# Performance work log

Hardware: AMD Instinct MI355X
Metric: run time of the kernel (lower is better)

## Reference

```python
import jax, jax.numpy as jnp
import numpy as np

B, S, D, H, Dh, A_N = 2, 1024, 512, 8, 64, 18
HID = H * Dh        # 512, equals in_features
FFN = 4 * D         # SwiGLU hidden (ratio=4)
EPS = 1e-6


def rmsnorm(x, scale):
    return x * jax.lax.rsqrt(jnp.mean(jnp.square(x), axis=-1, keepdims=True) + EPS) * scale


def setup_inputs() -> dict:
    key = jax.random.key(0)
    ks = jax.random.split(key, 16)
    lecun = lambda k, shp: jax.random.normal(k, shp, jnp.float32) * (1.0 / np.sqrt(shp[0]))
    return {
        "x": jax.random.normal(ks[0], (B, S, D), jnp.float32),
        "action": jax.random.randint(ks[1], (B, S), 0, A_N, jnp.int32),
        "mask": jnp.zeros((B, S), jnp.int32),
        "carry": jnp.zeros((B, H, Dh, Dh), jnp.float32),
        "norm1_scale": jnp.ones((D,), jnp.float32),
        "wq": lecun(ks[2], (D, HID)),
        "wk": lecun(ks[3], (D, HID)),
        "wv": lecun(ks[4], (D, HID)),
        "w_beta": lecun(ks[5], (D, H)),
        "embed": jax.random.normal(ks[6], (A_N, HID), jnp.float32) * 0.02,
        "w_alpha": lecun(ks[7], (HID, H)),
        "w_bu": lecun(ks[8], (HID, HID)),
        "w_bv": lecun(ks[9], (HID, HID)),
        "norm_attn_scale": jnp.ones((HID,), jnp.float32),
        "w_out": lecun(ks[10], (HID, D)),
        "b_out": jnp.zeros((D,), jnp.float32),
        "norm2_scale": jnp.ones((D,), jnp.float32),
        "w_gate": lecun(ks[11], (D, FFN)),
        "w_val": lecun(ks[12], (D, FFN)),
        "w_ffn": lecun(ks[13], (FFN, D)),
    }


def reference(x, action, mask, carry, norm1_scale, wq, wk, wv, w_beta, embed,
              w_alpha, w_bu, w_bv, norm_attn_scale, w_out, b_out,
              norm2_scale, w_gate, w_val, w_ffn):
    dt = x.dtype
    h = rmsnorm(x, norm1_scale)
    # projections -> [B,S,H,Dh]
    q = jax.nn.silu(h @ wq).reshape(B, S, H, Dh)
    k = jax.nn.silu(h @ wk).reshape(B, S, H, Dh)
    v = (h @ wv).reshape(B, S, H, Dh)
    beta = jax.nn.sigmoid(h @ w_beta)                       # [B,S,H]
    ae = embed[action]                                      # [B,S,HID]
    alpha = jax.nn.sigmoid(ae @ w_alpha)                    # [B,S,H]
    b_u = (ae @ w_bu).reshape(B, S, H, Dh)
    b_v = (ae @ w_bv).reshape(B, S, H, Dh)
    q = q / (jnp.linalg.norm(q, axis=-1, keepdims=True) + EPS)
    k = k / (jnp.linalg.norm(k, axis=-1, keepdims=True) + EPS)
    eye = jnp.eye(Dh, dtype=dt)
    # delta = I - beta * k k^T   -> [B,S,H,Dh,Dh]
    delta = eye - beta[..., None, None] * jnp.einsum("bshi,bshj->bshij", k, k)
    m = mask.astype(dt)[:, :, None, None, None]
    decay = alpha[..., None, None] * delta * (1.0 - m)
    drift = jnp.einsum("bshi,bshj->bshij", b_u, b_v)
    write = beta[..., None, None] * jnp.einsum("bshi,bshj->bshij", v, k)
    update = drift @ delta + write

    def binop(lhs, rhs):
        a_i, b_i = lhs
        a_j, b_j = rhs
        return (a_i @ a_j, b_i @ a_j + b_j)

    cumdecay, hs = jax.lax.associative_scan(jax.vmap(binop), (decay, update), axis=1)
    hs = carry[:, None] @ cumdecay + hs                     # [B,S,H,Dh,Dh]
    attn = jnp.einsum("bshij,bshj->bshi", hs, q).reshape(B, S, HID)
    attn = rmsnorm(attn, norm_attn_scale)
    y = attn @ w_out + b_out
    skip = y + x
    h2 = rmsnorm(skip, norm2_scale)
    ffn = (jax.nn.silu(h2 @ w_gate) * (h2 @ w_val)) @ w_ffn
    return (hs[:, -1], skip + ffn)
```

## Files before the change

### kernel.cpp

```cpp
#include <hip/hip_runtime.h>
#include <hip/hip_bf16.h>
#include <cstdint>
#include <cstddef>

using bf16 = __hip_bfloat16;
typedef __attribute__((ext_vector_type(8))) short bf16x8;
typedef __attribute__((ext_vector_type(4))) float f32x4;

static constexpr int B_ = 2, S_ = 1024, D_ = 512, H_ = 8;
static constexpr int M_ = B_ * S_;
static constexpr int CHUNKS_ = 64, CLEN_ = 16;
static constexpr float EPS_ = 1e-6f;

__device__ __forceinline__ float sigmoidf_(float x) { return 1.0f / (1.0f + __expf(-x)); }

__device__ __forceinline__ short bf_hi(float v, float& rem) {
  bf16 h = __float2bfloat16(v);
  rem = v - __bfloat162float(h);
  return *(short*)&h;
}
__device__ __forceinline__ short bf_of(float v) {
  bf16 h = __float2bfloat16(v);
  return *(short*)&h;
}

struct TJob { const float* src; bf16* dst; int K, N, base, xf; };
struct TTab { TJob j[9]; };

__global__ __launch_bounds__(256) void k_transpose_all(TTab tab) {
  __shared__ float tile[32][33];
  int blk = blockIdx.x;
  int ji = 0;
#pragma unroll
  for (int t = 1; t < 9; ++t) if (tab.j[t].base <= blk) ji = t;
  const float* W = tab.j[ji].src;
  bf16* Wt = tab.j[ji].dst;
  int K = tab.j[ji].K, N = tab.j[ji].N, xf = tab.j[ji].xf;
  int rel = blk - tab.j[ji].base;
  int nb = N >> 5;
  int n0 = (rel % nb) * 32, k0 = (rel / nb) * 32;
  int tx = threadIdx.x, ty = threadIdx.y;
#pragma unroll
  for (int r = ty; r < 32; r += 8) tile[r][tx] = W[(size_t)(k0 + r) * N + n0 + tx];
  __syncthreads();
#pragma unroll
  for (int r = ty; r < 32; r += 8) {
    int n = n0 + r;
    int drow = n;
    if (xf == 1) drow = ((n >> 5) << 6) + (n & 31);
    else if (xf == 2) drow = ((n >> 5) << 6) + (n & 31) + 32;
    Wt[(size_t)drow * K + k0 + tx] = __float2bfloat16(tile[tx][r]);
  }
}

__global__ __launch_bounds__(256) void k_pre(const float* __restrict__ x,
                                             const float* __restrict__ scale,
                                             float* __restrict__ hF, bf16* __restrict__ hB,
                                             const int* __restrict__ action,
                                             const float* __restrict__ embed,
                                             float* __restrict__ aeF, bf16* __restrict__ aeB) {
  int tid = threadIdx.x;
  if (blockIdx.x < M_) {
    int m = blockIdx.x;
    const float* row = x + (size_t)m * D_;
    float2 v = *(const float2*)(row + tid * 2);
    float ss = v.x * v.x + v.y * v.y;
#pragma unroll
    for (int o = 1; o < 64; o <<= 1) ss += __shfl_xor(ss, o);
    __shared__ float wsum[4];
    if ((tid & 63) == 0) wsum[tid >> 6] = ss;
    __syncthreads();
    float tot = wsum[0] + wsum[1] + wsum[2] + wsum[3];
    float rs = rsqrtf(tot * (1.0f / (float)D_) + EPS_);
    float2 sc = *(const float2*)(scale + tid * 2);
    float o0 = v.x * rs * sc.x, o1 = v.y * rs * sc.y;
    float2 o; o.x = o0; o.y = o1;
    *(float2*)(hF + (size_t)m * D_ + tid * 2) = o;
    bf16* p = hB + (size_t)m * D_ + tid * 2;
    p[0] = __float2bfloat16(o0); p[1] = __float2bfloat16(o1);
  } else {
    int m = blockIdx.x - M_;
    int a = action[m];
    float2 v = *(const float2*)(embed + (size_t)a * 512 + tid * 2);
    *(float2*)(aeF + (size_t)m * 512 + tid * 2) = v;
    bf16* p = aeB + (size_t)m * 512 + tid * 2;
    p[0] = __float2bfloat16(v.x); p[1] = __float2bfloat16(v.y);
  }
}

__global__ __launch_bounds__(256) void k_rmsnorm(const float* __restrict__ x,
                                                 const float* __restrict__ scale,
                                                 float* __restrict__ outf,
                                                 bf16* __restrict__ outb) {
  int m = blockIdx.x, tid = threadIdx.x;
  const float* row = x + (size_t)m * D_;
  float2 v = *(const float2*)(row + tid * 2);
  float ss = v.x * v.x + v.y * v.y;
#pragma unroll
  for (int o = 1; o < 64; o <<= 1) ss += __shfl_xor(ss, o);
  __shared__ float wsum[4];
  if ((tid & 63) == 0) wsum[tid >> 6] = ss;
  __syncthreads();
  float tot = wsum[0] + wsum[1] + wsum[2] + wsum[3];
  float rs = rsqrtf(tot * (1.0f / (float)D_) + EPS_);
  float2 sc = *(const float2*)(scale + tid * 2);
  float o0 = v.x * rs * sc.x, o1 = v.y * rs * sc.y;
  if (outf) {
    float2 o; o.x = o0; o.y = o1;
    *(float2*)(outf + (size_t)m * D_ + tid * 2) = o;
  }
  if (outb) {
    bf16* p = outb + (size_t)m * D_ + tid * 2;
    p[0] = __float2bfloat16(o0); p[1] = __float2bfloat16(o1);
  }
}

__global__ __launch_bounds__(256) void k_dot8x2(const float* __restrict__ hF,
                                                const float* __restrict__ aeF,
                                                const float* __restrict__ W1,
                                                const float* __restrict__ W2,
                                                float* __restrict__ o1,
                                                float* __restrict__ o2) {
  int m = blockIdx.x, tid = threadIdx.x;
  float x0 = hF[(size_t)m * D_ + tid], x1 = hF[(size_t)m * D_ + 256 + tid];
  float y0 = aeF[(size_t)m * D_ + tid], y1 = aeF[(size_t)m * D_ + 256 + tid];
  float p[8], q[8];
#pragma unroll
  for (int j = 0; j < 8; ++j) {
    p[j] = x0 * W1[tid * 8 + j] + x1 * W1[(tid + 256) * 8 + j];
    q[j] = y0 * W2[tid * 8 + j] + y1 * W2[(tid + 256) * 8 + j];
  }
#pragma unroll
  for (int j = 0; j < 8; ++j) {
#pragma unroll
    for (int o = 1; o < 64; o <<= 1) {
      p[j] += __shfl_xor(p[j], o);
      q[j] += __shfl_xor(q[j], o);
    }
  }
  __shared__ float sacc[4][16];
  if ((tid & 63) == 0) {
#pragma unroll
    for (int j = 0; j < 8; ++j) { sacc[tid >> 6][j] = p[j]; sacc[tid >> 6][8 + j] = q[j]; }
  }
  __syncthreads();
  if (tid < 8) {
    float s = sacc[0][tid] + sacc[1][tid] + sacc[2][tid] + sacc[3][tid];
    o1[(size_t)m * 8 + tid] = sigmoidf_(s);
  } else if (tid < 16) {
    int j = tid - 8;
    float s = sacc[0][8 + j] + sacc[1][8 + j] + sacc[2][8 + j] + sacc[3][8 + j];
    o2[(size_t)m * 8 + j] = sigmoidf_(s);
  }
}

__global__ __launch_bounds__(256) void k_qknorm_dots(float* __restrict__ qkv,
                                                     const float* __restrict__ buv,
                                                     const float* __restrict__ betaF,
                                                     const float* __restrict__ alphaF,
                                                     const int* __restrict__ mask,
                                                     float* __restrict__ scal8) {
  int blk = blockIdx.x * 4 + (threadIdx.x >> 6);
  int m = blk >> 3, h = blk & 7, t = threadIdx.x & 63;
  size_t qi = (size_t)m * 1536 + h * 64 + t;
  float q = qkv[qi], k = qkv[qi + 512];
  float bv = buv[(size_t)m * 1024 + 512 + h * 64 + t];
  float qs = q * q, ks = k * k;
#pragma unroll
  for (int o = 1; o < 64; o <<= 1) { qs += __shfl_xor(qs, o); ks += __shfl_xor(ks, o); }
  float qn = q / (sqrtf(qs) + EPS_);
  float kn = k / (sqrtf(ks) + EPS_);
  qkv[qi] = qn; qkv[qi + 512] = kn;
  float d0 = kn * qn, d1 = kn * bv, d2 = bv * qn;
#pragma unroll
  for (int o = 1; o < 64; o <<= 1) {
    d0 += __shfl_xor(d0, o); d1 += __shfl_xor(d1, o); d2 += __shfl_xor(d2, o);
  }
  if (t == 0) {
    int mh = m * 8 + h;
    float4 s4;
    s4.x = betaF[mh];
    s4.y = alphaF[mh] * (1.0f - (float)mask[m]);
    s4.z = d0; s4.w = d1;
    *(float4*)(scal8 + (size_t)mh * 8) = s4;
    scal8[(size_t)mh * 8 + 4] = d2;
  }
}

template <int EPI>
__global__ __launch_bounds__(256) void k_gemm2(const bf16* __restrict__ A,
                                               const bf16* __restrict__ Bt,
                                               void* __restrict__ Cv, int M, int N, int K,
                                               int actSplit, const float* __restrict__ bias,
                                               const float* __restrict__ res) {
  __shared__ bf16 As[2][64 * 32];
  __shared__ bf16 Bs[2][64 * 32];
  const int tid = threadIdx.x;
  const int wave = tid >> 6, lane = tid & 63;
  const int wm = wave >> 1, wn = wave & 1;
  const int m0 = blockIdx.y * 64, n0 = blockIdx.x * 64;
  const int lr = lane & 15, lg = lane >> 4;
  const int srow = (wave << 4) | (lane >> 2);
  const int skb = (lane & 3) << 3;
  const bf16* ga = A + (size_t)(m0 + srow) * K + skb;
  const bf16* gb = Bt + (size_t)(n0 + srow) * K + skb;

  f32x4 acc[2][2];
#pragma unroll
  for (int i = 0; i < 2; ++i)
#pragma unroll
    for (int j = 0; j < 2; ++j) acc[i][j] = (f32x4){0.f, 0.f, 0.f, 0.f};

  const int nk = K >> 5;
  int4 ar = *(const int4*)ga;
  int4 br = *(const int4*)gb;
  for (int t = 0; t < nk; ++t) {
    bf16* asb = &As[t & 1][0];
    bf16* bsb = &Bs[t & 1][0];
    *(int4*)(asb + tid * 8) = ar;
    *(int4*)(bsb + tid * 8) = br;
    __syncthreads();
    if (t + 1 < nk) {
      ar = *(const int4*)(ga + ((size_t)(t + 1) << 5));
      br = *(const int4*)(gb + ((size_t)(t + 1) << 5));
    }
    bf16x8 af[2], bfr[2];
#pragma unroll
    for (int mm = 0; mm < 2; ++mm)
      af[mm] = *(const bf16x8*)(asb + (wm * 32 + mm * 16 + lr) * 32 + lg * 8);
#pragma unroll
    for (int nn = 0; nn < 2; ++nn)
      bfr[nn] = *(const bf16x8*)(bsb + (wn * 32 + nn * 16 + lr) * 32 + lg * 8);
#pragma unroll
    for (int mm = 0; mm < 2; ++mm)
#pragma unroll
      for (int nn = 0; nn < 2; ++nn)
        acc[mm][nn] = __builtin_amdgcn_mfma_f32_16x16x32_bf16(af[mm], bfr[nn], acc[mm][nn], 0, 0, 0);
  }

  if constexpr (EPI == 4) {
    __syncthreads();
    float* gateL = (float*)&As[0][0];
    float* valL = (float*)&Bs[0][0];
    float* dstL = wn ? valL : gateL;
#pragma unroll
    for (int mm = 0; mm < 2; ++mm)
#pragma unroll
      for (int nn = 0; nn < 2; ++nn)
#pragma unroll
        for (int r = 0; r < 4; ++r)
          dstL[(wm * 32 + mm * 16 + lg * 4 + r) * 32 + nn * 16 + lr] = acc[mm][nn][r];
    __syncthreads();
    bf16* Cb = (bf16*)Cv;
    int row = tid >> 2, c0 = (tid & 3) * 8;
    bf16x8 o;
#pragma unroll
    for (int e = 0; e < 8; ++e) {
      float g = gateL[row * 32 + c0 + e];
      float v = valL[row * 32 + c0 + e];
      o[e] = bf_of(g * sigmoidf_(g) * v);
    }
    *(int4*)(Cb + (size_t)(m0 + row) * 2048 + blockIdx.x * 32 + c0) = *(int4*)&o;
  } else {
    float* C = (float*)Cv;
#pragma unroll
    for (int mm = 0; mm < 2; ++mm) {
#pragma unroll
      for (int nn = 0; nn < 2; ++nn) {
#pragma unroll
        for (int r = 0; r < 4; ++r) {
          int row = m0 + wm * 32 + mm * 16 + lg * 4 + r;
          int col = n0 + wn * 32 + nn * 16 + lr;
          float v = acc[mm][nn][r];
          if constexpr (EPI == 1) {
            if (col < actSplit) v = v * sigmoidf_(v);
          }
          if constexpr (EPI == 2) v += bias[col] + res[(size_t)row * N + col];
          if constexpr (EPI == 3) v += res[(size_t)row * N + col];
          C[(size_t)row * N + col] = v;
        }
      }
    }
  }
}


__global__ __launch_bounds__(512) void k_scan_chunk(
    const float* __restrict__ qkv, const float* __restrict__ buv,
    const float* __restrict__ scal8, bf16* __restrict__ PtHi,
    bf16* __restrict__ PtLo, float* __restrict__ Ut,
    float* __restrict__ Qtb, float* __restrict__ Vtb) {
  __shared__ float kL[CLEN_][64], qL[CLEN_][64], bvL[CLEN_][64];
  __shared__ float vL[CLEN_][64], buL[CLEN_][64];
  __shared__ float scL[CLEN_][8];
  const int blk = blockIdx.x, bh = blk >> 6, c = blk & (CHUNKS_ - 1);
  const int b = bh >> 3, h = bh & 7;
  const int tid = threadIdx.x, i = tid >> 3, q8 = tid & 7, j0 = q8 * 8;
  const bool writer = (q8 == 0);
  const int m0 = b * S_ + c * CLEN_;

  if (tid < 256) {
    int s = tid >> 4, fo = (tid & 15) * 4;
    const float* qb = qkv + (size_t)(m0 + s) * 1536 + h * 64;
    const float* bb = buv + (size_t)(m0 + s) * 1024 + h * 64;
    *(float4*)&qL[s][fo]  = *(const float4*)(qb + fo);
    *(float4*)&kL[s][fo]  = *(const float4*)(qb + 512 + fo);
    *(float4*)&vL[s][fo]  = *(const float4*)(qb + 1024 + fo);
    *(float4*)&buL[s][fo] = *(const float4*)(bb + fo);
    *(float4*)&bvL[s][fo] = *(const float4*)(bb + 512 + fo);
    if ((tid & 15) < 2)
      *(float4*)&scL[s][(tid & 1) * 4] =
          *(const float4*)(scal8 + (size_t)((m0 + s) * 8 + h) * 8 + (tid & 1) * 4);
  }
  __syncthreads();

  alignas(16) float P[8], U[8];
#pragma unroll
  for (int jj = 0; jj < 8; ++jj) { P[jj] = (j0 + jj == i) ? 1.f : 0.f; U[jj] = 0.f; }
  float* QT = Qtb + ((size_t)bh * CHUNKS_ + c) * (CLEN_ * 64);
  float* VT = Vtb + ((size_t)bh * CHUNKS_ + c) * (CLEN_ * 64);

  struct Step8 { float k[8], q[8], bv[8]; float v_i, bu_i, beta, g, kq, kbv, bvq; };
  auto LOAD = [&](Step8& sd, int s) {
    *(float4*)&sd.k[0]  = *(const float4*)&kL[s][j0];
    *(float4*)&sd.k[4]  = *(const float4*)&kL[s][j0 + 4];
    *(float4*)&sd.q[0]  = *(const float4*)&qL[s][j0];
    *(float4*)&sd.q[4]  = *(const float4*)&qL[s][j0 + 4];
    *(float4*)&sd.bv[0] = *(const float4*)&bvL[s][j0];
    *(float4*)&sd.bv[4] = *(const float4*)&bvL[s][j0 + 4];
    sd.v_i = vL[s][i];
    sd.bu_i = buL[s][i];
    float4 s4 = *(const float4*)&scL[s][0];
    sd.beta = s4.x; sd.g = s4.y; sd.kq = s4.z; sd.kbv = s4.w;
    sd.bvq = scL[s][4];
  };
  auto STEP = [&](const Step8& sd, int s) {
    float Pk = 0.f, Uk = 0.f, Pq = 0.f, Uq = 0.f;
#pragma unroll
    for (int jj = 0; jj < 8; ++jj) {
      Pk += P[jj] * sd.k[jj]; Uk += U[jj] * sd.k[jj];
      Pq += P[jj] * sd.q[jj]; Uq += U[jj] * sd.q[jj];
    }
    Pk += __shfl_xor(Pk, 1); Pk += __shfl_xor(Pk, 2); Pk += __shfl_xor(Pk, 4);
    Uk += __shfl_xor(Uk, 1); Uk += __shfl_xor(Uk, 2); Uk += __shfl_xor(Uk, 4);
    Pq += __shfl_xor(Pq, 1); Pq += __shfl_xor(Pq, 2); Pq += __shfl_xor(Pq, 4);
    Uq += __shfl_xor(Uq, 1); Uq += __shfl_xor(Uq, 2); Uq += __shfl_xor(Uq, 4);
    float gb = sd.g * sd.beta;
    float cP = gb * Pk;
    float Ai = sd.beta * sd.v_i - gb * Uk - sd.bu_i * sd.beta * sd.kbv;
    if (writer) {
      QT[s * 64 + i] = sd.g * Pq - cP * sd.kq;
      VT[s * 64 + i] = sd.g * Uq + Ai * sd.kq + sd.bu_i * sd.bvq;
    }
#pragma unroll
    for (int jj = 0; jj < 8; ++jj) {
      P[jj] = sd.g * P[jj] - cP * sd.k[jj];
      U[jj] = sd.g * U[jj] + Ai * sd.k[jj] + sd.bu_i * sd.bv[jj];
    }
  };

  Step8 A, Bs;
  LOAD(A, 0);
  LOAD(Bs, 1);
  for (int s = 0; s < CLEN_; s += 2) {
    STEP(A, s);
    if (s + 2 < CLEN_) LOAD(A, s + 2);
    STEP(Bs, s + 1);
    if (s + 3 < CLEN_) LOAD(Bs, s + 3);
  }

  const size_t base = ((size_t)bh * CHUNKS_ + c) * 4096;
#pragma unroll
  for (int jj = 0; jj < 8; ++jj) {
    int j = j0 + jj;
    float pv = P[jj];
    float rem;
    short ph = bf_hi(pv, rem);
    short pl = bf_of(rem);
    ((short*)PtHi)[base + (size_t)j * 64 + i] = ph;
    ((short*)PtLo)[base + (size_t)j * 64 + i] = pl;
    Ut[base + (size_t)j * 64 + i] = U[jj];
  }
}

#define PREFETCH_(SET, CIDX)                                                     \
  {                                                                              \
    const size_t cbo_ = (size_t)(CIDX) * 4096;                                   \
    _Pragma("unroll") for (int mt = 0; mt < 4; ++mt) {                           \
      _Pragma("unroll") for (int ks = 0; ks < 2; ++ks) {                         \
        size_t off_ = cbo_ + (size_t)(16 * mt + lr) * 64 + ks * 32 + lg * 8;     \
        aH[SET][mt][ks] = *(const bf16x8*)(PH + off_);                           \
        aL[SET][mt][ks] = *(const bf16x8*)(PL + off_);                           \
      }                                                                          \
      _Pragma("unroll") for (int r = 0; r < 4; ++r)                              \
        u[SET][mt][r] = UB[cbo_ + (size_t)(16 * mt + 4 * lg + r) * 64 + col0 + lr]; \
    }                                                                            \
  }

#define CHAINSTEP_(SET, NSET, CIDX)                                              \
  {                                                                              \
    if ((CIDX) + 1 < CHUNKS_) PREFETCH_(NSET, (CIDX) + 1);                       \
    _Pragma("unroll") for (int mt = 0; mt < 4; ++mt)                             \
      _Pragma("unroll") for (int r = 0; r < 4; ++r)                              \
        HB[(size_t)(CIDX) * 4096 + (size_t)(16 * mt + 4 * lg + r) * 64 + col0 + lr] = st[mt][r]; \
    bf16x8 bH[2], bL[2];                                                         \
    _Pragma("unroll") for (int ks = 0; ks < 2; ++ks) {                           \
      _Pragma("unroll") for (int e = 0; e < 8; ++e) {                            \
        int src_ = (2 * (lg & 1) + (e >> 2)) * 16 + lr;                          \
        float va_ = __shfl(st[2 * ks][e & 3], src_);                             \
        float vb_ = __shfl(st[2 * ks + 1][e & 3], src_);                         \
        float bv_ = (lg & 2) ? vb_ : va_;                                        \
        float rem_;                                                              \
        bH[ks][e] = bf_hi(bv_, rem_);                                            \
        bL[ks][e] = bf_of(rem_);                                                 \
      }                                                                          \
    }                                                                            \
    f32x4 stn[4];                                                                \
    _Pragma("unroll") for (int mt = 0; mt < 4; ++mt) {                           \
      f32x4 a_ = u[SET][mt];                                                     \
      _Pragma("unroll") for (int ks = 0; ks < 2; ++ks) {                         \
        a_ = __builtin_amdgcn_mfma_f32_16x16x32_bf16(aH[SET][mt][ks], bH[ks], a_, 0, 0, 0); \
        a_ = __builtin_amdgcn_mfma_f32_16x16x32_bf16(aH[SET][mt][ks], bL[ks], a_, 0, 0, 0); \
        a_ = __builtin_amdgcn_mfma_f32_16x16x32_bf16(aL[SET][mt][ks], bH[ks], a_, 0, 0, 0); \
      }                                                                          \
      stn[mt] = a_;                                                              \
    }                                                                            \
    _Pragma("unroll") for (int mt = 0; mt < 4; ++mt) st[mt] = stn[mt];           \
  }

__global__ __launch_bounds__(64, 1) void k_chain3(
    const bf16* __restrict__ PtHi, const bf16* __restrict__ PtLo,
    const float* __restrict__ Ut, const float* __restrict__ carry,
    float* __restrict__ Hbuf, float* __restrict__ out_hs) {
  const int bh = blockIdx.x >> 2, cb = blockIdx.x & 3, col0 = cb * 16;
  const int lane = threadIdx.x & 63, lr = lane & 15, lg = lane >> 4;
  const short* PH = (const short*)PtHi + (size_t)bh * CHUNKS_ * 4096;
  const short* PL = (const short*)PtLo + (size_t)bh * CHUNKS_ * 4096;
  const float* UB = Ut + (size_t)bh * CHUNKS_ * 4096;
  float* HB = Hbuf + (size_t)bh * CHUNKS_ * 4096;

  f32x4 st[4];
#pragma unroll
  for (int mt = 0; mt < 4; ++mt)
    st[mt] = *(const f32x4*)(carry + ((size_t)bh * 64 + col0 + lr) * 64 + 16 * mt + 4 * lg);

  bf16x8 aH[2][4][2], aL[2][4][2];
  f32x4 u[2][4];
  PREFETCH_(0, 0);
  for (int c = 0; c < CHUNKS_; c += 2) {
    CHAINSTEP_(0, 1, c);
    CHAINSTEP_(1, 0, c + 1);
  }
#pragma unroll
  for (int mt = 0; mt < 4; ++mt)
    *(f32x4*)(out_hs + ((size_t)bh * 64 + col0 + lr) * 64 + 16 * mt + 4 * lg) = st[mt];
}

__global__ __launch_bounds__(256) void k_attn_gemm(
    const float* __restrict__ Hbuf, const float* __restrict__ Qtb,
    const float* __restrict__ Vtb, float* __restrict__ attn) {
  const int blk = blockIdx.x, bh = blk >> 6, c = blk & (CHUNKS_ - 1);
  const int b = bh >> 3, h = bh & 7;
  const int tid = threadIdx.x, wave = tid >> 6, lane = tid & 63;
  const int lr = lane & 15, lg = lane >> 4;
  const float* H0 = Hbuf + ((size_t)bh * CHUNKS_ + c) * 4096;
  const float* QT = Qtb + ((size_t)bh * CHUNKS_ + c) * (CLEN_ * 64);
  const float* VT = Vtb + ((size_t)bh * CHUNKS_ + c) * (CLEN_ * 64);

  bf16x8 aH[2], aL[2];
#pragma unroll
  for (int ks = 0; ks < 2; ++ks) {
#pragma unroll
    for (int e = 0; e < 8; ++e) {
      float v = H0[(size_t)(ks * 32 + lg * 8 + e) * 64 + wave * 16 + lr];
      float rem;
      aH[ks][e] = bf_hi(v, rem);
      aL[ks][e] = bf_of(rem);
    }
  }
  f32x4 a = (f32x4){0.f, 0.f, 0.f, 0.f};
#pragma unroll
  for (int ks = 0; ks < 2; ++ks) {
    const float* qp = QT + (size_t)lr * 64 + ks * 32 + lg * 8;
    bf16x8 bH, bL;
#pragma unroll
    for (int e = 0; e < 8; ++e) {
      float rem;
      bH[e] = bf_hi(qp[e], rem);
      bL[e] = bf_of(rem);
    }
    a = __builtin_amdgcn_mfma_f32_16x16x32_bf16(aH[ks], bH, a, 0, 0, 0);
    a = __builtin_amdgcn_mfma_f32_16x16x32_bf16(aH[ks], bL, a, 0, 0, 0);
    a = __builtin_amdgcn_mfma_f32_16x16x32_bf16(aL[ks], bH, a, 0, 0, 0);
  }
  const int m0 = b * S_ + c * CLEN_;
  {
    int s = lr;
    f32x4 vt = *(const f32x4*)(VT + (size_t)s * 64 + wave * 16 + lg * 4);
#pragma unroll
    for (int r = 0; r < 4; ++r) a[r] += vt[r];
    *(f32x4*)(attn + (size_t)(m0 + s) * 512 + h * 64 + wave * 16 + lg * 4) = a;
  }
}

extern "C" void kernel_launch(void* const* d_in, const int* in_sizes, int n_in,
                              void* d_out, int out_size, void* d_ws, size_t ws_size,
                              hipStream_t stream) {
  const float* x      = (const float*)d_in[0];
  const int*   action = (const int*)d_in[1];
  const int*   mask   = (const int*)d_in[2];
  const float* carry  = (const float*)d_in[3];
  const float* n1s    = (const float*)d_in[4];
  const float* wq     = (const float*)d_in[5];
  const float* wk     = (const float*)d_in[6];
  const float* wv     = (const float*)d_in[7];
  const float* wbeta  = (const float*)d_in[8];
  const float* embed  = (const float*)d_in[9];
  const float* walpha = (const float*)d_in[10];
  const float* wbu    = (const float*)d_in[11];
  const float* wbv    = (const float*)d_in[12];
  const float* nas    = (const float*)d_in[13];
  const float* wout   = (const float*)d_in[14];
  const float* bout   = (const float*)d_in[15];
  const float* n2s    = (const float*)d_in[16];
  const float* wgate  = (const float*)d_in[17];
  const float* wval   = (const float*)d_in[18];
  const float* wffn   = (const float*)d_in[19];

  float* out_hs  = (float*)d_out;
  float* out_ffn = (float*)d_out + 65536;

  char* p = (char*)d_ws;
  auto alloc = [&](size_t bytes) -> char* {
    char* r = p; p += (bytes + 255) & ~(size_t)255; return r;
  };
  bf16*  wqkvT = (bf16*)alloc((size_t)1536 * 512 * 2);
  bf16*  wbuvT = (bf16*)alloc((size_t)1024 * 512 * 2);
  bf16*  woutT = (bf16*)alloc((size_t)512 * 512 * 2);
  bf16*  wgvT  = (bf16*)alloc((size_t)4096 * 512 * 2);
  bf16*  wffnT = (bf16*)alloc((size_t)512 * 2048 * 2);
  float* qkvF  = (float*)alloc((size_t)M_ * 1536 * 4);
  float* buvF  = (float*)alloc((size_t)M_ * 1024 * 4);
  float* betaF = (float*)alloc((size_t)M_ * 8 * 4);
  float* alphaF= (float*)alloc((size_t)M_ * 8 * 4);
  float* scal8 = (float*)alloc((size_t)M_ * 8 * 8 * 4);
  float* attnF = (float*)alloc((size_t)M_ * 512 * 4);
  bf16*  attnB = (bf16*)alloc((size_t)M_ * 512 * 2);
  float* skipF = (float*)alloc((size_t)M_ * 512 * 4);
  bf16*  h2B   = (bf16*)alloc((size_t)M_ * 512 * 2);
  bf16*  ffnB  = (bf16*)alloc((size_t)M_ * 2048 * 2);
  char*  tail  = alloc((size_t)32 * 1024 * 1024);
  if ((size_t)(p - (char*)d_ws) > ws_size) return;

  float* hF  = (float*)tail;
  bf16*  hB  = (bf16*)(tail + ((size_t)4 << 20));
  float* aeF = (float*)(tail + ((size_t)6 << 20));
  bf16*  aeB = (bf16*)(tail + ((size_t)10 << 20));

  bf16*  PtHi = (bf16*)tail;
  bf16*  PtLo = (bf16*)(tail + ((size_t)8 << 20));
  float* UtB  = (float*)(tail + ((size_t)16 << 20));
  float* Hbuf = qkvF;
  float* Qtb  = (float*)attnB;
  float* Vtb  = (float*)((char*)skipF + ((size_t)2 << 20));

  TTab tab;
  tab.j[0] = {wq,    wqkvT,              512,  512,  0,    0};
  tab.j[1] = {wk,    wqkvT + 512 * 512,  512,  512,  256,  0};
  tab.j[2] = {wv,    wqkvT + 1024 * 512, 512,  512,  512,  0};
  tab.j[3] = {wbu,   wbuvT,              512,  512,  768,  0};
  tab.j[4] = {wbv,   wbuvT + 512 * 512,  512,  512,  1024, 0};
  tab.j[5] = {wout,  woutT,              512,  512,  1280, 0};
  tab.j[6] = {wgate, wgvT,               512,  2048, 1536, 1};
  tab.j[7] = {wval,  wgvT,               512,  2048, 2560, 2};
  tab.j[8] = {wffn,  wffnT,              2048, 512,  3584, 0};
  k_transpose_all<<<4608, dim3(32, 8), 0, stream>>>(tab);

  k_pre<<<M_ * 2, 256, 0, stream>>>(x, n1s, hF, hB, action, embed, aeF, aeB);

  k_gemm2<1><<<dim3(1536 / 64, M_ / 64), 256, 0, stream>>>(hB, wqkvT, qkvF, M_, 1536, 512, 1024, nullptr, nullptr);
  k_gemm2<0><<<dim3(1024 / 64, M_ / 64), 256, 0, stream>>>(aeB, wbuvT, buvF, M_, 1024, 512, 0, nullptr, nullptr);
  k_dot8x2<<<M_, 256, 0, stream>>>(hF, aeF, wbeta, walpha, betaF, alphaF);
  k_qknorm_dots<<<M_ * 2, 256, 0, stream>>>(qkvF, buvF, betaF, alphaF, mask, scal8);

  k_scan_chunk<<<16 * CHUNKS_, 512, 0, stream>>>(qkvF, buvF, scal8, PtHi, PtLo, UtB, Qtb, Vtb);
  k_chain3<<<64, 64, 0, stream>>>(PtHi, PtLo, UtB, carry, Hbuf, out_hs);
  k_attn_gemm<<<16 * CHUNKS_, 256, 0, stream>>>(Hbuf, Qtb, Vtb, attnF);

  k_rmsnorm<<<M_, 256, 0, stream>>>(attnF, nas, nullptr, attnB);
  k_gemm2<2><<<dim3(512 / 64, M_ / 64), 256, 0, stream>>>(attnB, woutT, skipF, M_, 512, 512, 0, bout, x);
  k_rmsnorm<<<M_, 256, 0, stream>>>(skipF, n2s, nullptr, h2B);
  k_gemm2<4><<<dim3(4096 / 64, M_ / 64), 256, 0, stream>>>(h2B, wgvT, ffnB, M_, 4096, 512, 0, nullptr, nullptr);
  k_gemm2<3><<<dim3(512 / 64, M_ / 64), 256, 0, stream>>>(ffnB, wffnT, out_ffn, M_, 512, 2048, 0, nullptr, skipF);
}
```

Baseline: 221.8 us.

## Use 16x16x16 MFMA in chain kernel to drop cross-lane shuffles

```diff
diff --git a/kernel.cpp b/kernel.cpp
--- a/kernel.cpp
+++ b/kernel.cpp
@@ -5,6 +5,7 @@
 
 using bf16 = __hip_bfloat16;
 typedef __attribute__((ext_vector_type(8))) short bf16x8;
+typedef __attribute__((ext_vector_type(4))) short short4v;
 typedef __attribute__((ext_vector_type(4))) float f32x4;
 
 static constexpr int B_ = 2, S_ = 1024, D_ = 512, H_ = 8;
@@ -383,77 +384,83 @@
   }
 }
 
-#define PREFETCH_(SET, CIDX)                                                     \
-  {                                                                              \
-    const size_t cbo_ = (size_t)(CIDX) * 4096;                                   \
-    _Pragma("unroll") for (int mt = 0; mt < 4; ++mt) {                           \
-      _Pragma("unroll") for (int ks = 0; ks < 2; ++ks) {                         \
-        size_t off_ = cbo_ + (size_t)(16 * mt + lr) * 64 + ks * 32 + lg * 8;     \
-        aH[SET][mt][ks] = *(const bf16x8*)(PH + off_);                           \
-        aL[SET][mt][ks] = *(const bf16x8*)(PL + off_);                           \
-      }                                                                          \
-      _Pragma("unroll") for (int r = 0; r < 4; ++r)                              \
-        u[SET][mt][r] = UB[cbo_ + (size_t)(16 * mt + 4 * lg + r) * 64 + col0 + lr]; \
-    }                                                                            \
-  }
-
-#define CHAINSTEP_(SET, NSET, CIDX)                                              \
-  {                                                                              \
-    if ((CIDX) + 1 < CHUNKS_) PREFETCH_(NSET, (CIDX) + 1);                       \
-    _Pragma("unroll") for (int mt = 0; mt < 4; ++mt)                             \
-      _Pragma("unroll") for (int r = 0; r < 4; ++r)                              \
-        HB[(size_t)(CIDX) * 4096 + (size_t)(16 * mt + 4 * lg + r) * 64 + col0 + lr] = st[mt][r]; \
-    bf16x8 bH[2], bL[2];                                                         \
-    _Pragma("unroll") for (int ks = 0; ks < 2; ++ks) {                           \
-      _Pragma("unroll") for (int e = 0; e < 8; ++e) {                            \
-        int src_ = (2 * (lg & 1) + (e >> 2)) * 16 + lr;                          \
-        float va_ = __shfl(st[2 * ks][e & 3], src_);                             \
-        float vb_ = __shfl(st[2 * ks + 1][e & 3], src_);                         \
-        float bv_ = (lg & 2) ? vb_ : va_;                                        \
-        float rem_;                                                              \
-        bH[ks][e] = bf_hi(bv_, rem_);                                            \
-        bL[ks][e] = bf_of(rem_);                                                 \
-      }                                                                          \
-    }                                                                            \
-    f32x4 stn[4];                                                                \
-    _Pragma("unroll") for (int mt = 0; mt < 4; ++mt) {                           \
-      f32x4 a_ = u[SET][mt];                                                     \
-      _Pragma("unroll") for (int ks = 0; ks < 2; ++ks) {                         \
-        a_ = __builtin_amdgcn_mfma_f32_16x16x32_bf16(aH[SET][mt][ks], bH[ks], a_, 0, 0, 0); \
-        a_ = __builtin_amdgcn_mfma_f32_16x16x32_bf16(aH[SET][mt][ks], bL[ks], a_, 0, 0, 0); \
-        a_ = __builtin_amdgcn_mfma_f32_16x16x32_bf16(aL[SET][mt][ks], bH[ks], a_, 0, 0, 0); \
-      }                                                                          \
-      stn[mt] = a_;                                                              \
-    }                                                                            \
-    _Pragma("unroll") for (int mt = 0; mt < 4; ++mt) st[mt] = stn[mt];           \
-  }
-
-__global__ __launch_bounds__(64, 1) void k_chain3(
+#define MFMA16_(Af, Bf, Cf) __builtin_amdgcn_mfma_f32_16x16x16bf16_1k(Af, Bf, Cf, 0, 0, 0)
+
+#define PF16_(SET, CIDX)                                                       \
+  {                                                                            \
+    const size_t pbo_ = (size_t)(CIDX) * 4096;                                 \
+    _Pragma("unroll") for (int mt = 0; mt < 4; ++mt)                           \
+      _Pragma("unroll") for (int kt = 0; kt < 4; ++kt) {                       \
+        size_t off_ = pbo_ + (size_t)(16 * mt + lr) * 64 + 16 * kt + 4 * lg;   \
+        aH[SET][mt][kt] = *(const short4v*)(PH + off_);                        \
+        aL[SET][mt][kt] = *(const short4v*)(PL + off_);                        \
+      }                                                                        \
+  }
+
+#define CS16_(SET, NSET, CIDX)                                                 \
+  {                                                                            \
+    if ((CIDX) + 1 < CHUNKS_) PF16_(NSET, (CIDX) + 1);                         \
+    const size_t cbo_ = (size_t)(CIDX) * 4096;                                 \
+    f32x4 u_[2][4];                                                            \
+    _Pragma("unroll") for (int ct = 0; ct < 2; ++ct)                           \
+      _Pragma("unroll") for (int mt = 0; mt < 4; ++mt)                         \
+        _Pragma("unroll") for (int r = 0; r < 4; ++r)                          \
+          u_[ct][mt][r] = UB[cbo_ + (size_t)(16 * mt + 4 * lg + r) * 64 + col0 + 16 * ct + lr]; \
+    short4v bH[2][4], bL[2][4];                                                \
+    _Pragma("unroll") for (int ct = 0; ct < 2; ++ct)                           \
+      _Pragma("unroll") for (int kt = 0; kt < 4; ++kt)                         \
+        _Pragma("unroll") for (int e = 0; e < 4; ++e) {                        \
+          float rem_;                                                          \
+          bH[ct][kt][e] = bf_hi(st[ct][kt][e], rem_);                          \
+          bL[ct][kt][e] = bf_of(rem_);                                         \
+        }                                                                      \
+    _Pragma("unroll") for (int ct = 0; ct < 2; ++ct)                           \
+      _Pragma("unroll") for (int kt = 0; kt < 4; ++kt)                         \
+        _Pragma("unroll") for (int r = 0; r < 4; ++r)                          \
+          HB[cbo_ + (size_t)(16 * kt + 4 * lg + r) * 64 + col0 + 16 * ct + lr] = st[ct][kt][r]; \
+    _Pragma("unroll") for (int ct = 0; ct < 2; ++ct)                           \
+      _Pragma("unroll") for (int mt = 0; mt < 4; ++mt) {                       \
+        f32x4 a_ = u_[ct][mt];                                                 \
+        _Pragma("unroll") for (int kt = 0; kt < 4; ++kt) {                     \
+          a_ = MFMA16_(aH[SET][mt][kt], bH[ct][kt], a_);                       \
+          a_ = MFMA16_(aH[SET][mt][kt], bL[ct][kt], a_);                       \
+          a_ = MFMA16_(aL[SET][mt][kt], bH[ct][kt], a_);                       \
+        }                                                                      \
+        st[ct][mt] = a_;                                                       \
+      }                                                                        \
+  }
+
+__global__ __launch_bounds__(64, 1) void k_chain4(
     const bf16* __restrict__ PtHi, const bf16* __restrict__ PtLo,
     const float* __restrict__ Ut, const float* __restrict__ carry,
     float* __restrict__ Hbuf, float* __restrict__ out_hs) {
-  const int bh = blockIdx.x >> 2, cb = blockIdx.x & 3, col0 = cb * 16;
+  const int bh = blockIdx.x >> 1, half = blockIdx.x & 1, col0 = half * 32;
   const int lane = threadIdx.x & 63, lr = lane & 15, lg = lane >> 4;
   const short* PH = (const short*)PtHi + (size_t)bh * CHUNKS_ * 4096;
   const short* PL = (const short*)PtLo + (size_t)bh * CHUNKS_ * 4096;
   const float* UB = Ut + (size_t)bh * CHUNKS_ * 4096;
   float* HB = Hbuf + (size_t)bh * CHUNKS_ * 4096;
 
-  f32x4 st[4];
-#pragma unroll
-  for (int mt = 0; mt < 4; ++mt)
-    st[mt] = *(const f32x4*)(carry + ((size_t)bh * 64 + col0 + lr) * 64 + 16 * mt + 4 * lg);
-
-  bf16x8 aH[2][4][2], aL[2][4][2];
-  f32x4 u[2][4];
-  PREFETCH_(0, 0);
+  f32x4 st[2][4];
+#pragma unroll
+  for (int ct = 0; ct < 2; ++ct)
+#pragma unroll
+    for (int kt = 0; kt < 4; ++kt)
+      st[ct][kt] = *(const f32x4*)(carry +
+          ((size_t)bh * 64 + col0 + 16 * ct + lr) * 64 + 16 * kt + 4 * lg);
+
+  short4v aH[2][4][4], aL[2][4][4];
+  PF16_(0, 0);
   for (int c = 0; c < CHUNKS_; c += 2) {
-    CHAINSTEP_(0, 1, c);
-    CHAINSTEP_(1, 0, c + 1);
-  }
-#pragma unroll
-  for (int mt = 0; mt < 4; ++mt)
-    *(f32x4*)(out_hs + ((size_t)bh * 64 + col0 + lr) * 64 + 16 * mt + 4 * lg) = st[mt];
+    CS16_(0, 1, c);
+    CS16_(1, 0, c + 1);
+  }
+#pragma unroll
+  for (int ct = 0; ct < 2; ++ct)
+#pragma unroll
+    for (int kt = 0; kt < 4; ++kt)
+      *(f32x4*)(out_hs + ((size_t)bh * 64 + col0 + 16 * ct + lr) * 64 + 16 * kt + 4 * lg) =
+          st[ct][kt];
 }
 
 __global__ __launch_bounds__(256) void k_attn_gemm(
@@ -584,7 +591,7 @@
   k_qknorm_dots<<<M_ * 2, 256, 0, stream>>>(qkvF, buvF, betaF, alphaF, mask, scal8);
 
   k_scan_chunk<<<16 * CHUNKS_, 512, 0, stream>>>(qkvF, buvF, scal8, PtHi, PtLo, UtB, Qtb, Vtb);
-  k_chain3<<<64, 64, 0, stream>>>(PtHi, PtLo, UtB, carry, Hbuf, out_hs);
+  k_chain4<<<32, 64, 0, stream>>>(PtHi, PtLo, UtB, carry, Hbuf, out_hs);
   k_attn_gemm<<<16 * CHUNKS_, 256, 0, stream>>>(Hbuf, Qtb, Vtb, attnF);
 
   k_rmsnorm<<<M_, 256, 0, stream>>>(attnF, nas, nullptr, attnB);
```

After: 394.6 us. 1.78x slower.
